# Kernel optimization log

Measured on AMD Instinct MI355X. Metric: run time of the kernel, lower is better.

## Reference

```python
import jax, jax.numpy as jnp
import numpy as np

B, S, D, H, N = 4, 2048, 512, 8, 64
HD = D // H  # head dim


def setup_inputs() -> dict:
    key = jax.random.key(0)
    ks = jax.random.split(key, 4)
    s = 0.02  # xavier-ish init scale
    return {
        "x": jax.random.normal(ks[0], (B, S, D), jnp.float32),
        "in_proj_w": jax.random.normal(ks[1], (3 * D, D), jnp.float32) * s,
        "in_proj_b": jnp.zeros((3 * D,), jnp.float32),
        "out_proj_w": jax.random.normal(ks[2], (D, D), jnp.float32) * s,
        "out_proj_b": jnp.zeros((D,), jnp.float32),
        "content_w": jax.random.normal(ks[3], (N, D), jnp.float32) * s,
        "content_b": jnp.zeros((N,), jnp.float32),
        "k_input": 16,
    }


def _fwd_core(x, in_proj_w, in_proj_b, out_proj_w, out_proj_b, content_w, content_b):
    # torch nn.MultiheadAttention (batch_first, eval/no dropout), self-attention
    qkv = jnp.einsum("bsd,ed->bse", x, in_proj_w) + in_proj_b  # [B,S,3D]
    q, k, v = jnp.split(qkv, 3, axis=-1)
    to_heads = lambda t: t.reshape(B, S, H, HD).transpose(0, 2, 1, 3)  # [B,H,S,hd]
    q, k, v = to_heads(q), to_heads(k), to_heads(v)
    scores = jnp.einsum("bhqd,bhkd->bhqk", q, k) / jnp.sqrt(jnp.float32(HD))
    attn = jax.nn.softmax(scores, axis=-1)  # [B,H,S,S] (need_weights=True path)
    ctx = jnp.einsum("bhqk,bhkd->bhqd", attn, v)
    ctx = ctx.transpose(0, 2, 1, 3).reshape(B, S, D)
    attended = jnp.einsum("bsd,ed->bse", ctx, out_proj_w) + out_proj_b  # [B,S,D]

    # content_to_neuron
    aff = jnp.einsum("bsd,nd->bsn", attended, content_w) + content_b  # [B,S,N]

    # position importance: mean over heads, sum over keys, normalize
    pos_imp = attn.mean(axis=1).sum(axis=2)  # [B,S]
    pos_imp = pos_imp / (pos_imp.sum(axis=1, keepdims=True) + 1e-8)

    weighted = (aff * pos_imp[..., None]).sum(axis=1)  # [B,N]
    final = 0.5 * weighted + 0.3 * aff.max(axis=1) + 0.2 * aff.mean(axis=1)
    probs = jax.nn.softmax(final, axis=-1)
    return final, probs, attended


def reference(x, in_proj_w, in_proj_b, out_proj_w, out_proj_b, content_w, content_b, k_input):
    final, probs, attended = _fwd_core(
        x, in_proj_w, in_proj_b, out_proj_w, out_proj_b, content_w, content_b
    )
    _, input_idx = jax.lax.top_k(final, k_input)  # [B,k]
    one_hot = jnp.zeros_like(probs).at[jnp.arange(B)[:, None], input_idx].set(1.0)
    # straight-through: value == one_hot, gradient flows through probs
    routing_weights = jax.lax.stop_gradient(one_hot - probs) + probs
    return input_idx, routing_weights, attended
```

## Files before the change

### kernel.cpp

```cpp
#include <hip/hip_runtime.h>
#include <hip/hip_bf16.h>

typedef unsigned short u16;
typedef __bf16 bf16x8 __attribute__((ext_vector_type(8)));
typedef u16 u16x8 __attribute__((ext_vector_type(8)));
typedef u16 u16x4 __attribute__((ext_vector_type(4)));
typedef float f32x4 __attribute__((ext_vector_type(4)));

__device__ __forceinline__ u16 f2bf(float f) {
  union { float f; unsigned u; } v; v.f = f;
  return (u16)((v.u + 0x7FFFu + ((v.u >> 16) & 1u)) >> 16);
}
__device__ __forceinline__ float bf2f(u16 h) {
  union { unsigned u; float f; } v; v.u = ((unsigned)h) << 16;
  return v.f;
}
struct BfPair { u16 hi, lo; };
__device__ __forceinline__ BfPair split2(float f) {
  BfPair r;
  r.hi = f2bf(f);
  r.lo = f2bf(f - bf2f(r.hi));
  return r;
}
__device__ __forceinline__ bf16x8 as_bf16x8(u16x8 u) {
  union { u16x8 u; bf16x8 b; } v; v.u = u; return v.b;
}

#define MFMA16(a, b, c) __builtin_amdgcn_mfma_f32_16x16x32_bf16((a), (b), (c), 0, 0, 0)

__global__ __launch_bounds__(256) void split_kernel(
    const float* __restrict__ src, u16* __restrict__ hi, u16* __restrict__ lo, int n4)
{
  int i = blockIdx.x * 256 + threadIdx.x;
  if (i >= n4) return;
  f32x4 v = ((const f32x4*)src)[i];
  u16x4 h, l;
  #pragma unroll
  for (int j = 0; j < 4; j++) { BfPair p = split2(v[j]); h[j] = p.hi; l[j] = p.lo; }
  ((u16x4*)hi)[i] = h;
  ((u16x4*)lo)[i] = l;
}

template<int OUT_PLANES>
__global__ __launch_bounds__(256) void gemm_nt(
    const u16* __restrict__ Ah, const u16* __restrict__ Al,
    const u16* __restrict__ Bh, const u16* __restrict__ Bl,
    const float* __restrict__ bias,
    void* __restrict__ C0, void* __restrict__ C1,
    int M, int N, int K)
{
  constexpr int PAD = 56;
  __shared__ u16 Ash[64 * PAD];
  __shared__ u16 Asl[64 * PAD];
  __shared__ u16 Bsh[64 * PAD];
  __shared__ u16 Bsl[64 * PAD];
  const int t = threadIdx.x;
  const int lane = t & 63, w = t >> 6;
  const int m0 = blockIdx.x * 64, n0 = blockIdx.y * 64;
  const int srow = t >> 2;
  const int sc8 = (t & 3) * 8;

  f32x4 acc[4] = {};
  u16x8 avh, avl, bvh, bvl;

  {
    size_t ia = (size_t)(m0 + srow) * K + sc8;
    size_t ib = (size_t)(n0 + srow) * K + sc8;
    avh = *(const u16x8*)(Ah + ia); avl = *(const u16x8*)(Al + ia);
    bvh = *(const u16x8*)(Bh + ib); bvl = *(const u16x8*)(Bl + ib);
  }

  for (int k0 = 0; k0 < K; k0 += 32) {
    __syncthreads();
    *(u16x8*)&Ash[srow * PAD + sc8] = avh;
    *(u16x8*)&Asl[srow * PAD + sc8] = avl;
    *(u16x8*)&Bsh[srow * PAD + sc8] = bvh;
    *(u16x8*)&Bsl[srow * PAD + sc8] = bvl;
    if (k0 + 32 < K) {
      size_t ia = (size_t)(m0 + srow) * K + k0 + 32 + sc8;
      size_t ib = (size_t)(n0 + srow) * K + k0 + 32 + sc8;
      avh = *(const u16x8*)(Ah + ia); avl = *(const u16x8*)(Al + ia);
      bvh = *(const u16x8*)(Bh + ib); bvl = *(const u16x8*)(Bl + ib);
    }
    __syncthreads();
    bf16x8 ah = *(const bf16x8*)&Ash[(w * 16 + (lane & 15)) * PAD + (lane >> 4) * 8];
    bf16x8 al = *(const bf16x8*)&Asl[(w * 16 + (lane & 15)) * PAD + (lane >> 4) * 8];
    #pragma unroll
    for (int cb = 0; cb < 4; cb++) {
      bf16x8 bh = *(const bf16x8*)&Bsh[(cb * 16 + (lane & 15)) * PAD + (lane >> 4) * 8];
      bf16x8 bl = *(const bf16x8*)&Bsl[(cb * 16 + (lane & 15)) * PAD + (lane >> 4) * 8];
      acc[cb] = MFMA16(ah, bh, acc[cb]);
      acc[cb] = MFMA16(ah, bl, acc[cb]);
      acc[cb] = MFMA16(al, bh, acc[cb]);
    }
  }

  const int r0 = m0 + w * 16 + (lane >> 4) * 4;
  const int cl = lane & 15;
  #pragma unroll
  for (int cb = 0; cb < 4; cb++) {
    const int col = n0 + cb * 16 + cl;
    const float bs = bias[col];
    #pragma unroll
    for (int r = 0; r < 4; r++) {
      float v = acc[cb][r] + bs;
      size_t idx = (size_t)(r0 + r) * N + col;
      if (OUT_PLANES) {
        BfPair pp = split2(v);
        ((u16*)C0)[idx] = pp.hi;
        ((u16*)C1)[idx] = pp.lo;
      } else {
        ((float*)C0)[idx] = v;
      }
    }
  }
}

__global__ __launch_bounds__(256, 2) void attn_kernel(
    const u16* __restrict__ qkv_h, const u16* __restrict__ qkv_l,
    u16* __restrict__ ctx_h, u16* __restrict__ ctx_l)
{
  const int bh = blockIdx.x;
  const int b = bh >> 3, h = bh & 7;
  const int q0 = blockIdx.y * 128;
  const int t = threadIdx.x, lane = t & 63, w = t >> 6;
  const int l15 = lane & 15, g = lane >> 4;

  __shared__ u16 Ksh[64 * 72], Ksl[64 * 72];
  __shared__ u16 Vsh[64 * 72], Vsl[64 * 72];
  __shared__ u16 Psh[4][32 * 72], Psl[4][32 * 72];

  const size_t rowbase = (size_t)b * 2048;

  bf16x8 qbh[2][2], qbl[2][2];
  #pragma unroll
  for (int i = 0; i < 2; i++) {
    size_t qoff = (rowbase + q0 + i * 64 + w * 16 + l15) * 1536 + h * 64 + g * 8;
    #pragma unroll
    for (int kc = 0; kc < 2; kc++) {
      u16x8 uh = *(const u16x8*)(qkv_h + qoff + kc * 32);
      u16x8 ul = *(const u16x8*)(qkv_l + qoff + kc * 32);
      #pragma unroll
      for (int j = 0; j < 8; j++) {
        uh[j] = f2bf(bf2f(uh[j]) * 0.125f);
        ul[j] = f2bf(bf2f(ul[j]) * 0.125f);
      }
      qbh[i][kc] = as_bf16x8(uh);
      qbl[i][kc] = as_bf16x8(ul);
    }
  }

  f32x4 oacc[2][4] = {};
  float l_q[2] = {0.f, 0.f};

  u16x8 skh[2], skl[2], svh[2], svl[2];
  #pragma unroll
  for (int rep = 0; rep < 2; rep++) {
    int c = t + rep * 256;
    int row = c >> 3, col = (c & 7) * 8;
    size_t off = (rowbase + row) * 1536 + h * 64 + col;
    skh[rep] = *(const u16x8*)(qkv_h + off + 512);
    skl[rep] = *(const u16x8*)(qkv_l + off + 512);
    svh[rep] = *(const u16x8*)(qkv_h + off + 1024);
    svl[rep] = *(const u16x8*)(qkv_l + off + 1024);
  }

  for (int kt = 0; kt < 32; kt++) {
    __syncthreads();
    #pragma unroll
    for (int rep = 0; rep < 2; rep++) {
      int c = t + rep * 256;
      int row = c >> 3, col = (c & 7) * 8;
      *(u16x8*)&Ksh[row * 72 + col] = skh[rep];
      *(u16x8*)&Ksl[row * 72 + col] = skl[rep];
      int rk = (row + col) & 63;
      #pragma unroll
      for (int j = 0; j < 8; j++) {
        Vsh[(col + j) * 72 + rk] = svh[rep][j];
        Vsl[(col + j) * 72 + rk] = svl[rep][j];
      }
    }
    if (kt + 1 < 32) {
      #pragma unroll
      for (int rep = 0; rep < 2; rep++) {
        int c = t + rep * 256;
        int row = c >> 3, col = (c & 7) * 8;
        size_t off = (rowbase + (kt + 1) * 64 + row) * 1536 + h * 64 + col;
        skh[rep] = *(const u16x8*)(qkv_h + off + 512);
        skl[rep] = *(const u16x8*)(qkv_l + off + 512);
        svh[rep] = *(const u16x8*)(qkv_h + off + 1024);
        svl[rep] = *(const u16x8*)(qkv_l + off + 1024);
      }
    }
    __syncthreads();

    f32x4 sa0[4] = {}, sa1[4] = {};
    #pragma unroll
    for (int kc = 0; kc < 2; kc++) {
      #pragma unroll
      for (int cb = 0; cb < 4; cb++) {
        int ki = (cb * 16 + l15) * 72 + g * 8 + kc * 32;
        bf16x8 kh = *(const bf16x8*)&Ksh[ki];
        bf16x8 kl = *(const bf16x8*)&Ksl[ki];
        sa0[cb] = MFMA16(kh, qbh[0][kc], sa0[cb]);
        sa1[cb] = MFMA16(kh, qbh[1][kc], sa1[cb]);
        sa0[cb] = MFMA16(kh, qbl[0][kc], sa0[cb]);
        sa1[cb] = MFMA16(kh, qbl[1][kc], sa1[cb]);
        sa0[cb] = MFMA16(kl, qbh[0][kc], sa0[cb]);
        sa1[cb] = MFMA16(kl, qbh[1][kc], sa1[cb]);
      }
    }

    #pragma unroll
    for (int i = 0; i < 2; i++) {
      f32x4* sa = (i == 0) ? sa0 : sa1;
      float rs = 0.f;
      #pragma unroll
      for (int cb = 0; cb < 4; cb++)
        #pragma unroll
        for (int r = 0; r < 4; r++) {
          float p = __expf(sa[cb][r]);
          sa[cb][r] = p;
          rs += p;
        }
      rs += __shfl_xor(rs, 16, 64);
      rs += __shfl_xor(rs, 32, 64);
      l_q[i] += rs;

      #pragma unroll
      for (int cb = 0; cb < 4; cb++) {
        u16x4 ph, pl;
        #pragma unroll
        for (int r = 0; r < 4; r++) {
          BfPair pp = split2(sa[cb][r]);
          ph[r] = pp.hi; pl[r] = pp.lo;
        }
        int pi = (i * 16 + l15) * 72 + cb * 16 + g * 4;
        *(u16x4*)&Psh[w][pi] = ph;
        *(u16x4*)&Psl[w][pi] = pl;
      }
    }

    asm volatile("s_waitcnt lgkmcnt(0)" ::: "memory");
    __builtin_amdgcn_sched_barrier(0);

    bf16x8 pah[2][2], pal[2][2];
    #pragma unroll
    for (int i = 0; i < 2; i++)
      #pragma unroll
      for (int kc = 0; kc < 2; kc++) {
        int pb = (i * 16 + l15) * 72 + kc * 32 + g * 8;
        pah[i][kc] = *(const bf16x8*)&Psh[w][pb];
        pal[i][kc] = *(const bf16x8*)&Psl[w][pb];
      }

    #pragma unroll
    for (int kc = 0; kc < 2; kc++) {
      #pragma unroll
      for (int cb = 0; cb < 4; cb++) {
        int d = cb * 16 + l15;
        int rk0 = (g * 8 + kc * 32 + (d & 56)) & 63;
        bf16x8 vbh = *(const bf16x8*)&Vsh[d * 72 + rk0];
        bf16x8 vbl = *(const bf16x8*)&Vsl[d * 72 + rk0];
        oacc[0][cb] = MFMA16(pah[0][kc], vbh, oacc[0][cb]);
        oacc[1][cb] = MFMA16(pah[1][kc], vbh, oacc[1][cb]);
        oacc[0][cb] = MFMA16(pah[0][kc], vbl, oacc[0][cb]);
        oacc[1][cb] = MFMA16(pah[1][kc], vbl, oacc[1][cb]);
        oacc[0][cb] = MFMA16(pal[0][kc], vbh, oacc[0][cb]);
        oacc[1][cb] = MFMA16(pal[1][kc], vbh, oacc[1][cb]);
      }
    }
  }

  #pragma unroll
  for (int i = 0; i < 2; i++)
    #pragma unroll
    for (int r = 0; r < 4; r++) {
      float lq = __shfl(l_q[i], g * 4 + r, 64);
      float inv = 1.0f / lq;
      int row = q0 + i * 64 + w * 16 + g * 4 + r;
      size_t base = (rowbase + row) * 512 + h * 64;
      #pragma unroll
      for (int cb = 0; cb < 4; cb++) {
        BfPair pp = split2(oacc[i][cb][r] * inv);
        ctx_h[base + cb * 16 + l15] = pp.hi;
        ctx_l[base + cb * 16 + l15] = pp.lo;
      }
    }
}

__global__ __launch_bounds__(256) void aff_reduce(
    const float* __restrict__ att, const float* __restrict__ cw,
    const float* __restrict__ cbias, float* __restrict__ psum, float* __restrict__ pmax)
{
  const int b = blockIdx.x, sb = blockIdx.y;
  const int t = threadIdx.x;
  const int n = t & 63, rg = t >> 6;
  __shared__ float cws[64 * 65];
  __shared__ float ats[32 * 65];
  __shared__ float reds[256], redm[256];

  float acc[8] = {};
  for (int kc = 0; kc < 8; kc++) {
    __syncthreads();
    #pragma unroll
    for (int i = 0; i < 4; i++) {
      int c = t + i * 256;
      int row = c >> 4, col = (c & 15) * 4;
      f32x4 v = *(const f32x4*)(cw + (size_t)row * 512 + kc * 64 + col);
      cws[row * 65 + col + 0] = v[0]; cws[row * 65 + col + 1] = v[1];
      cws[row * 65 + col + 2] = v[2]; cws[row * 65 + col + 3] = v[3];
    }
    #pragma unroll
    for (int i = 0; i < 2; i++) {
      int c = t + i * 256;
      int row = c >> 4, col = (c & 15) * 4;
      f32x4 v = *(const f32x4*)(att + ((size_t)b * 2048 + sb * 32 + row) * 512 + kc * 64 + col);
      ats[row * 65 + col + 0] = v[0]; ats[row * 65 + col + 1] = v[1];
      ats[row * 65 + col + 2] = v[2]; ats[row * 65 + col + 3] = v[3];
    }
    __syncthreads();
    for (int k = 0; k < 64; k++) {
      float c = cws[n * 65 + k];
      #pragma unroll
      for (int r = 0; r < 8; r++)
        acc[r] += ats[(rg * 8 + r) * 65 + k] * c;
    }
  }
  const float bn = cbias[n];
  float s = 0.f, m = -1e30f;
  #pragma unroll
  for (int r = 0; r < 8; r++) {
    float v = acc[r] + bn;
    s += v; m = fmaxf(m, v);
  }
  reds[t] = s; redm[t] = m;
  __syncthreads();
  if (t < 64) {
    float ss = reds[t] + reds[64 + t] + reds[128 + t] + reds[192 + t];
    float mm = fmaxf(fmaxf(redm[t], redm[64 + t]), fmaxf(redm[128 + t], redm[192 + t]));
    psum[((size_t)b * 64 + sb) * 64 + t] = ss;
    pmax[((size_t)b * 64 + sb) * 64 + t] = mm;
  }
}

__global__ void final_topk(const float* __restrict__ psum, const float* __restrict__ pmax,
                           float* __restrict__ out)
{
  __shared__ float fin[4][64];
  const int t = threadIdx.x;
  const int b = t >> 6, n = t & 63;
  float s = 0.f, m = -1e30f;
  for (int j = 0; j < 64; j++) {
    s += psum[((size_t)b * 64 + j) * 64 + n];
    m = fmaxf(m, pmax[((size_t)b * 64 + j) * 64 + n]);
  }
  const float mean = s * (1.0f / 2048.0f);
  fin[b][n] = 0.5f * mean + 0.3f * m + 0.2f * mean;
  __syncthreads();
  if (t < 4) {
    unsigned long long chosen = 0ull;
    for (int j = 0; j < 16; j++) {
      float best = -3e38f; int bi = 0;
      for (int nn = 0; nn < 64; nn++) {
        float v = fin[t][nn];
        if (!((chosen >> nn) & 1ull) && v > best) { best = v; bi = nn; }
      }
      chosen |= 1ull << bi;
      out[t * 16 + j] = (float)bi;
    }
    for (int nn = 0; nn < 64; nn++)
      out[64 + t * 64 + nn] = ((chosen >> nn) & 1ull) ? 1.0f : 0.0f;
  }
}

extern "C" void kernel_launch(void* const* d_in, const int* in_sizes, int n_in,
                              void* d_out, int out_size, void* d_ws, size_t ws_size,
                              hipStream_t stream) {
  const float* x    = (const float*)d_in[0];
  const float* win  = (const float*)d_in[1];
  const float* bin  = (const float*)d_in[2];
  const float* wout = (const float*)d_in[3];
  const float* bout = (const float*)d_in[4];
  const float* cw   = (const float*)d_in[5];
  const float* cbv  = (const float*)d_in[6];
  (void)in_sizes; (void)n_in; (void)ws_size; (void)out_size;

  float* out = (float*)d_out;
  char* ws = (char*)d_ws;
  u16*   qkv_h = (u16*)ws;
  u16*   qkv_l = (u16*)(ws + 25165824);
  u16*   ctx_h = (u16*)(ws + 50331648);
  u16*   ctx_l = (u16*)(ws + 58720256);
  float* psum  = (float*)(ws + 67108864);
  float* pmax  = (float*)(ws + 67174400);
  u16*   winh  = (u16*)(ws + 67239936);
  u16*   winl  = (u16*)(ws + 68812800);
  u16*   wouth = (u16*)(ws + 70385664);
  u16*   woutl = (u16*)(ws + 70909952);
  u16*   xh = ctx_h, *xl = ctx_l;
  float* attended = out + 320;

  split_kernel<<<4096, 256, 0, stream>>>(x, xh, xl, 1048576);
  split_kernel<<<768, 256, 0, stream>>>(win, winh, winl, 196608);
  split_kernel<<<256, 256, 0, stream>>>(wout, wouth, woutl, 65536);

  gemm_nt<1><<<dim3(128, 24), 256, 0, stream>>>(
      xh, xl, winh, winl, bin, qkv_h, qkv_l, 8192, 1536, 512);
  attn_kernel<<<dim3(32, 16), 256, 0, stream>>>(qkv_h, qkv_l, ctx_h, ctx_l);
  gemm_nt<0><<<dim3(128, 8), 256, 0, stream>>>(
      ctx_h, ctx_l, wouth, woutl, bout, attended, nullptr, 8192, 512, 512);
  aff_reduce<<<dim3(4, 64), 256, 0, stream>>>(attended, cw, cbv, psum, pmax);
  final_topk<<<1, 256, 0, stream>>>(psum, pmax, out);
}
```

Baseline: 289.9 us.

## Enlarge GEMM tiles to 128x128 with direct global-to-LDS loads and XOR swizzle

Rewrites the split-bf16 GEMM to compute 128x128 output tiles per block, with each wave owning a 64x64 sub-tile of 4x4 MFMA accumulators. The tile grows from 64x64 to raise operand reuse per LDS load. Operands are now copied with global_load_lds straight into LDS, which replaces the register-staged prefetch. An XOR swizzle replaces the padding to avoid bank conflicts. Because the software prefetch is gone, global loads no longer overlap compute within a block. The out-projection grid also shrinks to 256 blocks, which may leave CUs underused.

Result: faster. 283.6 us (-2.2%).

```diff
diff --git a/kernel.cpp b/kernel.cpp
--- a/kernel.cpp
+++ b/kernel.cpp
@@ -27,6 +27,11 @@
 }
 
 #define MFMA16(a, b, c) __builtin_amdgcn_mfma_f32_16x16x32_bf16((a), (b), (c), 0, 0, 0)
+
+#define GLD16(gp, lp)                                                          \
+  __builtin_amdgcn_global_load_lds(                                            \
+      (const __attribute__((address_space(1))) void*)(gp),                     \
+      (__attribute__((address_space(3))) void*)(lp), 16, 0, 0)
 
 __global__ __launch_bounds__(256) void split_kernel(
     const float* __restrict__ src, u16* __restrict__ hi, u16* __restrict__ lo, int n4)
@@ -42,78 +47,89 @@
 }
 
 template<int OUT_PLANES>
-__global__ __launch_bounds__(256) void gemm_nt(
+__global__ __launch_bounds__(256, 3) void gemm_nt(
     const u16* __restrict__ Ah, const u16* __restrict__ Al,
     const u16* __restrict__ Bh, const u16* __restrict__ Bl,
     const float* __restrict__ bias,
     void* __restrict__ C0, void* __restrict__ C1,
     int M, int N, int K)
 {
-  constexpr int PAD = 56;
-  __shared__ u16 Ash[64 * PAD];
-  __shared__ u16 Asl[64 * PAD];
-  __shared__ u16 Bsh[64 * PAD];
-  __shared__ u16 Bsl[64 * PAD];
+  __shared__ u16 Ash[128 * 32], Asl[128 * 32];
+  __shared__ u16 Bsh[128 * 32], Bsl[128 * 32];
   const int t = threadIdx.x;
   const int lane = t & 63, w = t >> 6;
-  const int m0 = blockIdx.x * 64, n0 = blockIdx.y * 64;
-  const int srow = t >> 2;
-  const int sc8 = (t & 3) * 8;
-
-  f32x4 acc[4] = {};
-  u16x8 avh, avl, bvh, bvl;
-
-  {
-    size_t ia = (size_t)(m0 + srow) * K + sc8;
-    size_t ib = (size_t)(n0 + srow) * K + sc8;
-    avh = *(const u16x8*)(Ah + ia); avl = *(const u16x8*)(Al + ia);
-    bvh = *(const u16x8*)(Bh + ib); bvl = *(const u16x8*)(Bl + ib);
-  }
+  const int l15 = lane & 15, g = lane >> 4;
+  const int m0 = blockIdx.x * 128, n0 = blockIdx.y * 128;
+
+  const int lrow = lane >> 2;
+  const int lchunk = lane & 3;
+
+  f32x4 acc[4][4] = {};
 
   for (int k0 = 0; k0 < K; k0 += 32) {
     __syncthreads();
-    *(u16x8*)&Ash[srow * PAD + sc8] = avh;
-    *(u16x8*)&Asl[srow * PAD + sc8] = avl;
-    *(u16x8*)&Bsh[srow * PAD + sc8] = bvh;
-    *(u16x8*)&Bsl[srow * PAD + sc8] = bvl;
-    if (k0 + 32 < K) {
-      size_t ia = (size_t)(m0 + srow) * K + k0 + 32 + sc8;
-      size_t ib = (size_t)(n0 + srow) * K + k0 + 32 + sc8;
-      avh = *(const u16x8*)(Ah + ia); avl = *(const u16x8*)(Al + ia);
-      bvh = *(const u16x8*)(Bh + ib); bvl = *(const u16x8*)(Bl + ib);
-    }
-    __syncthreads();
-    bf16x8 ah = *(const bf16x8*)&Ash[(w * 16 + (lane & 15)) * PAD + (lane >> 4) * 8];
-    bf16x8 al = *(const bf16x8*)&Asl[(w * 16 + (lane & 15)) * PAD + (lane >> 4) * 8];
-    #pragma unroll
-    for (int cb = 0; cb < 4; cb++) {
-      bf16x8 bh = *(const bf16x8*)&Bsh[(cb * 16 + (lane & 15)) * PAD + (lane >> 4) * 8];
-      bf16x8 bl = *(const bf16x8*)&Bsl[(cb * 16 + (lane & 15)) * PAD + (lane >> 4) * 8];
-      acc[cb] = MFMA16(ah, bh, acc[cb]);
-      acc[cb] = MFMA16(ah, bl, acc[cb]);
-      acc[cb] = MFMA16(al, bh, acc[cb]);
-    }
-  }
-
-  const int r0 = m0 + w * 16 + (lane >> 4) * 4;
-  const int cl = lane & 15;
-  #pragma unroll
-  for (int cb = 0; cb < 4; cb++) {
-    const int col = n0 + cb * 16 + cl;
-    const float bs = bias[col];
-    #pragma unroll
-    for (int r = 0; r < 4; r++) {
-      float v = acc[cb][r] + bs;
-      size_t idx = (size_t)(r0 + r) * N + col;
-      if (OUT_PLANES) {
-        BfPair pp = split2(v);
-        ((u16*)C0)[idx] = pp.hi;
-        ((u16*)C1)[idx] = pp.lo;
-      } else {
-        ((float*)C0)[idx] = v;
-      }
-    }
-  }
+    #pragma unroll
+    for (int q = 0; q < 2; q++) {
+      const int row = w * 32 + q * 16 + lrow;
+      const int sw = lchunk ^ (row & 3) ^ ((row >> 2) & 3);
+      const size_t ga = (size_t)(m0 + row) * K + k0 + sw * 8;
+      const size_t gb = (size_t)(n0 + row) * K + k0 + sw * 8;
+      const int ldsbase = (w * 32 + q * 16) * 32;
+      GLD16(Ah + ga, &Ash[ldsbase]);
+      GLD16(Al + ga, &Asl[ldsbase]);
+      GLD16(Bh + gb, &Bsh[ldsbase]);
+      GLD16(Bl + gb, &Bsl[ldsbase]);
+    }
+    __syncthreads();
+
+    bf16x8 bh[4], bl[4];
+    #pragma unroll
+    for (int n = 0; n < 4; n++) {
+      const int row = (w & 1) * 64 + n * 16 + l15;
+      const int slot = g ^ (row & 3) ^ ((row >> 2) & 3);
+      const int idx = row * 32 + slot * 8;
+      bh[n] = *(const bf16x8*)&Bsh[idx];
+      bl[n] = *(const bf16x8*)&Bsl[idx];
+    }
+    #pragma unroll
+    for (int m = 0; m < 4; m++) {
+      const int row = (w >> 1) * 64 + m * 16 + l15;
+      const int slot = g ^ (row & 3) ^ ((row >> 2) & 3);
+      const int idx = row * 32 + slot * 8;
+      bf16x8 ah = *(const bf16x8*)&Ash[idx];
+      bf16x8 al = *(const bf16x8*)&Asl[idx];
+      #pragma unroll
+      for (int n = 0; n < 4; n++) {
+        acc[m][n] = MFMA16(ah, bh[n], acc[m][n]);
+        acc[m][n] = MFMA16(ah, bl[n], acc[m][n]);
+        acc[m][n] = MFMA16(al, bh[n], acc[m][n]);
+      }
+    }
+  }
+
+  const int r0 = m0 + (w >> 1) * 64;
+  const int c0 = n0 + (w & 1) * 64;
+  float bs[4];
+  #pragma unroll
+  for (int n = 0; n < 4; n++) bs[n] = bias[c0 + n * 16 + l15];
+  #pragma unroll
+  for (int m = 0; m < 4; m++)
+    #pragma unroll
+    for (int n = 0; n < 4; n++) {
+      const int col = c0 + n * 16 + l15;
+      #pragma unroll
+      for (int r = 0; r < 4; r++) {
+        float v = acc[m][n][r] + bs[n];
+        size_t idx = (size_t)(r0 + m * 16 + g * 4 + r) * N + col;
+        if (OUT_PLANES) {
+          BfPair pp = split2(v);
+          ((u16*)C0)[idx] = pp.hi;
+          ((u16*)C1)[idx] = pp.lo;
+        } else {
+          ((float*)C0)[idx] = v;
+        }
+      }
+    }
 }
 
 __global__ __launch_bounds__(256, 2) void attn_kernel(
@@ -405,10 +421,10 @@
   split_kernel<<<768, 256, 0, stream>>>(win, winh, winl, 196608);
   split_kernel<<<256, 256, 0, stream>>>(wout, wouth, woutl, 65536);
 
-  gemm_nt<1><<<dim3(128, 24), 256, 0, stream>>>(
+  gemm_nt<1><<<dim3(64, 12), 256, 0, stream>>>(
       xh, xl, winh, winl, bin, qkv_h, qkv_l, 8192, 1536, 512);
   attn_kernel<<<dim3(32, 16), 256, 0, stream>>>(qkv_h, qkv_l, ctx_h, ctx_l);
-  gemm_nt<0><<<dim3(128, 8), 256, 0, stream>>>(
+  gemm_nt<0><<<dim3(64, 4), 256, 0, stream>>>(
       ctx_h, ctx_l, wouth, woutl, bout, attended, nullptr, 8192, 512, 512);
   aff_reduce<<<dim3(4, 64), 256, 0, stream>>>(attended, cw, cbv, psum, pmax);
   final_topk<<<1, 256, 0, stream>>>(psum, pmax, out);
```
